# Performance work log

Hardware: AMD Instinct MI355X
Metric: run time of the kernel (lower is better)

Reference implementation:

```python
import jax, jax.numpy as jnp
import numpy as np

N = 50000      # nodes
E = 800000     # directed edges (avg degree 16)
F_IN = 128     # input_size
HID = 128      # hidden_size
OUT = 64       # output_size (bottleneck)
EPS = 1e-5     # BatchNorm eps


def setup_inputs() -> dict:
    key = jax.random.key(0)
    ks = jax.random.split(key, 8)
    x = jax.random.normal(ks[0], (N, F_IN), dtype=jnp.float32)
    edge_index = jax.random.randint(ks[1], (2, E), 0, N, dtype=jnp.int64)
    dims = [(F_IN, HID), (HID, HID), (HID, OUT),   # encoder
            (OUT, HID), (HID, HID), (HID, F_IN)]   # decoder
    wkeys = jax.random.split(ks[2], 6)
    inp = {"x": x, "edge_index": edge_index}
    for j, (fi, fo) in enumerate(dims):
        inp[f"W{j}"] = jax.random.normal(wkeys[j], (fi, fo), dtype=jnp.float32) / np.sqrt(fi).astype(np.float32)
        inp[f"b{j}"] = jnp.zeros((fo,), dtype=jnp.float32)
        inp[f"g{j}"] = jnp.ones((fo,), dtype=jnp.float32)   # BN gamma
        inp[f"be{j}"] = jnp.zeros((fo,), dtype=jnp.float32)  # BN beta
    return inp


def _gcn(x, W, b, src, dst, edge_norm, inv_deg):
    # GCNConv: x' = D^-1/2 (A+I) D^-1/2 (x W) + b, sum-aggregation over edges
    h = x @ W                                   # [N, Fo]
    msg = h[src] * edge_norm[:, None]            # [E, Fo] gather + scale
    agg = jax.ops.segment_sum(msg, dst, num_segments=N)  # scatter-add
    agg = agg + h * inv_deg[:, None]             # self-loop term (norm = 1/deg)
    return agg + b


def _bn(x, g, be):
    # BatchNorm1d over nodes, training-mode batch statistics (biased var)
    m = jnp.mean(x, axis=0)
    v = jnp.mean((x - m) ** 2, axis=0)
    return (x - m) * jax.lax.rsqrt(v + EPS) * g + be


def _forward(x, edge_index, Ws, bs, gs, bes):
    src, dst = edge_index[0], edge_index[1]
    # degrees with self-loops (GCN adds self-loops, counts incoming edges)
    deg = jnp.zeros((N,), dtype=x.dtype).at[dst].add(1.0) + 1.0
    dinv_sqrt = jax.lax.rsqrt(deg)
    edge_norm = dinv_sqrt[src] * dinv_sqrt[dst]
    inv_deg = 1.0 / deg
    h = x
    for j in range(6):
        h = _gcn(h, Ws[j], bs[j], src, dst, edge_norm, inv_deg)
        h = _bn(h, gs[j], bes[j])
        if j not in (2, 5):  # ReLU after first two layers of each GNN, not after bn3
            h = jax.nn.relu(h)
    return h


def reference(x, edge_index,
              W0, b0, g0, be0, W1, b1, g1, be1, W2, b2, g2, be2,
              W3, b3, g3, be3, W4, b4, g4, be4, W5, b5, g5, be5):
    Ws = (W0, W1, W2, W3, W4, W5)
    bs = (b0, b1, b2, b3, b4, b5)
    gs = (g0, g1, g2, g3, g4, g5)
    bes = (be0, be1, be2, be3, be4, be5)
    return _forward(x, edge_index, Ws, bs, gs, bes)
```

## Files before the change

kernel.cpp:

```cpp
#include <hip/hip_runtime.h>
#include <hip/hip_bf16.h>

#define N_NODES 50000
#define N_EDGES 800000
constexpr float BN_EPS = 1e-5f;
constexpr int NCHUNK = (N_NODES + 1023) / 1024;

typedef unsigned short ushortT;

__device__ __forceinline__ unsigned short f2bf(float f) {
    __hip_bfloat16 h = __float2bfloat16(f);
    return __builtin_bit_cast(unsigned short, h);
}
__device__ __forceinline__ void cvt4(uint2 v, float* f) {
    f[0] = __uint_as_float(v.x << 16); f[1] = __uint_as_float(v.x & 0xffff0000u);
    f[2] = __uint_as_float(v.y << 16); f[3] = __uint_as_float(v.y & 0xffff0000u);
}


__global__ void count_deg(const int* __restrict__ dst, int* cnts) {
    int e = blockIdx.x * 256 + threadIdx.x;
    if (e < N_EDGES) atomicAdd(&cnts[dst[e]], 1);
}

__global__ void finalize_deg(const int* __restrict__ cnts, float* __restrict__ dinv,
                             float* __restrict__ invdeg) {
    int i = blockIdx.x * 256 + threadIdx.x;
    if (i < N_NODES) {
        float d = (float)cnts[i] + 1.0f;
        dinv[i] = rsqrtf(d);
        invdeg[i] = 1.0f / d;
    }
}

__global__ __launch_bounds__(256)
void scan_block_sums(const int* __restrict__ counts, int* __restrict__ totals) {
    __shared__ int red[4];
    int tid = threadIdx.x;
    int base = blockIdx.x * 1024 + tid * 4;
    int s = 0;
    #pragma unroll
    for (int j = 0; j < 4; ++j) { int i = base + j; if (i < N_NODES) s += counts[i]; }
    #pragma unroll
    for (int d = 1; d < 64; d <<= 1) s += __shfl_xor(s, d, 64);
    if ((tid & 63) == 0) red[tid >> 6] = s;
    __syncthreads();
    if (tid == 0) totals[blockIdx.x] = red[0] + red[1] + red[2] + red[3];
}

__global__ __launch_bounds__(256)
void scan_write(const int* __restrict__ counts, const int* __restrict__ totals,
                int* __restrict__ offs, int* __restrict__ cursor) {
    __shared__ int chunkbase;
    __shared__ int wsum[4];
    int tid = threadIdx.x, lane = tid & 63, wid = tid >> 6;
    if (tid == 0) { int a = 0; for (int i = 0; i < (int)blockIdx.x; ++i) a += totals[i]; chunkbase = a; }
    int base = blockIdx.x * 1024 + tid * 4;
    int v[4]; int s = 0;
    #pragma unroll
    for (int j = 0; j < 4; ++j) { int i = base + j; v[j] = (i < N_NODES) ? counts[i] : 0; s += v[j]; }
    int ts = s;
    #pragma unroll
    for (int d = 1; d < 64; d <<= 1) { int t = __shfl_up(ts, d, 64); if (lane >= d) ts += t; }
    if (lane == 63) wsum[wid] = ts;
    __syncthreads();
    int wbase = 0;
    #pragma unroll
    for (int w = 0; w < 4; ++w) if (w < wid) wbase += wsum[w];
    int excl = chunkbase + wbase + (ts - s);
    #pragma unroll
    for (int j = 0; j < 4; ++j) {
        int i = base + j;
        if (i < N_NODES) { offs[i] = excl; cursor[i] = excl; }
        excl += v[j];
    }
}

__global__ void fill_csr(const int* __restrict__ src, const int* __restrict__ dst,
                         const float* __restrict__ dinv, int* cursor,
                         uint2* __restrict__ edges) {
    int e = blockIdx.x * 256 + threadIdx.x;
    if (e < N_EDGES) {
        int s = src[e], d = dst[e];
        int pos = atomicAdd(&cursor[d], 1);
        edges[pos] = make_uint2((unsigned)s, __float_as_uint(dinv[s] * dinv[d]));
    }
}


template<int FI, int FO, bool BN, bool RELU>
__global__ __launch_bounds__(256)
void gemm_bn(const float* __restrict__ X, const float* __restrict__ W,
             ushortT* __restrict__ Hb, const float* __restrict__ stats_prev,
             const float* __restrict__ g_prev, const float* __restrict__ be_prev) {
    constexpr int CT = FO / 4;
    constexpr int RT = 256 / CT;
    constexpr int ROWS = RT * 4;
    __shared__ ushortT Ws[FI * FO];
    __shared__ float xs[ROWS * FI];
    __shared__ float sscale[FI], sshift[FI];
    if constexpr (BN) {
        if (threadIdx.x < FI) {
            constexpr float invN = 1.0f / (float)N_NODES;
            int k = threadIdx.x;
            float m = stats_prev[k] * invN;
            float var = stats_prev[FI + k] * invN - m * m;
            float is = rsqrtf(var + BN_EPS) * g_prev[k];
            sscale[k] = is;
            sshift[k] = be_prev[k] - m * is;
        }
    }
    for (int i = threadIdx.x * 8; i < FI * FO; i += 256 * 8) {
        float4 w0 = *(const float4*)&W[i];
        float4 w1 = *(const float4*)&W[i + 4];
        ushortT us[8] = { f2bf(w0.x), f2bf(w0.y), f2bf(w0.z), f2bf(w0.w),
                          f2bf(w1.x), f2bf(w1.y), f2bf(w1.z), f2bf(w1.w) };
        *(uint4*)&Ws[i] = *(uint4*)us;
    }
    const int ct = threadIdx.x % CT, rt = threadIdx.x / CT;
    const int col = ct * 4;
    ushortT* Hcol = Hb + (size_t)(col >> 5) * N_NODES * 32 + (col & 31);
    const int ntiles = (N_NODES + ROWS - 1) / ROWS;
    for (int tile = blockIdx.x; tile < ntiles; tile += gridDim.x) {
        const int base = tile * ROWS;
        __syncthreads();
        for (int t = threadIdx.x; t < ROWS * FI / 4; t += 256) {
            int r = t / (FI / 4), k4 = (t % (FI / 4)) * 4;
            int gr = base + r;
            float4 v = (gr < N_NODES) ? *(const float4*)&X[(size_t)gr * FI + k4]
                                      : make_float4(0.f, 0.f, 0.f, 0.f);
            if constexpr (BN) {
                float4 sc = *(const float4*)&sscale[k4];
                float4 sh = *(const float4*)&sshift[k4];
                v.x = fmaf(v.x, sc.x, sh.x); v.y = fmaf(v.y, sc.y, sh.y);
                v.z = fmaf(v.z, sc.z, sh.z); v.w = fmaf(v.w, sc.w, sh.w);
                if constexpr (RELU) {
                    v.x = fmaxf(v.x, 0.f); v.y = fmaxf(v.y, 0.f);
                    v.z = fmaxf(v.z, 0.f); v.w = fmaxf(v.w, 0.f);
                }
            }
            *(float4*)&xs[r * FI + k4] = v;
        }
        __syncthreads();
        float acc[4][4] = {};
        #pragma unroll 2
        for (int k4 = 0; k4 < FI; k4 += 4) {
            float4 xv[4], wv[4];
            #pragma unroll
            for (int ri = 0; ri < 4; ++ri)
                xv[ri] = *(const float4*)&xs[(rt * 4 + ri) * FI + k4];
            #pragma unroll
            for (int j = 0; j < 4; ++j) {
                ushort4 wu = *(const ushort4*)&Ws[(k4 + j) * FO + col];
                wv[j] = make_float4(__uint_as_float((unsigned)wu.x << 16),
                                    __uint_as_float((unsigned)wu.y << 16),
                                    __uint_as_float((unsigned)wu.z << 16),
                                    __uint_as_float((unsigned)wu.w << 16));
            }
            #pragma unroll
            for (int ri = 0; ri < 4; ++ri) {
                #pragma unroll
                for (int j = 0; j < 4; ++j) {
                    float xk = ((const float*)&xv[ri])[j];
                    acc[ri][0] = fmaf(xk, wv[j].x, acc[ri][0]);
                    acc[ri][1] = fmaf(xk, wv[j].y, acc[ri][1]);
                    acc[ri][2] = fmaf(xk, wv[j].z, acc[ri][2]);
                    acc[ri][3] = fmaf(xk, wv[j].w, acc[ri][3]);
                }
            }
        }
        #pragma unroll
        for (int ri = 0; ri < 4; ++ri) {
            int row = base + rt * 4 + ri;
            if (row < N_NODES) {
                ushortT us[4] = { f2bf(acc[ri][0]), f2bf(acc[ri][1]),
                                  f2bf(acc[ri][2]), f2bf(acc[ri][3]) };
                *(ushort4*)&Hcol[(size_t)row * 32] = *(ushort4*)us;
            }
        }
    }
}


template<int FO>
__global__ __launch_bounds__(256)
void aggregate_sliced(const ushortT* __restrict__ Hb, const int* __restrict__ offs,
                      const int* __restrict__ cnt, const uint2* __restrict__ edges,
                      const float* __restrict__ invdeg, const float* __restrict__ bias,
                      float* __restrict__ out, float* __restrict__ stats) {
    constexpr int NPASS = FO / 32;
    constexpr int BPX = 8 / NPASS;
    const int b = blockIdx.x;
    const int pass = (b & 7) / BPX;
    const int bi = (b >> 3) * BPX + (b & 7) % BPX;
    const int NBP = gridDim.x / NPASS;
    const int lt = threadIdx.x & 7;
    const int sub = threadIdx.x >> 3;
    const uint2* S2 = (const uint2*)(Hb + (size_t)pass * N_NODES * 32);
    const int f0 = pass * 32 + lt * 4;
    float bb[4] = { bias[f0], bias[f0 + 1], bias[f0 + 2], bias[f0 + 3] };
    float s[4] = {}, s2[4] = {};
    for (int r = bi * 32 + sub; r < N_NODES; r += NBP * 32) {
        float idg = invdeg[r];
        float a[4], f[4];
        cvt4(S2[(size_t)r * 8 + lt], f);
        #pragma unroll
        for (int j = 0; j < 4; ++j) a[j] = fmaf(f[j], idg, bb[j]);
        int e = offs[r], en = e + cnt[r];
        for (; e < en; ++e) {
            uint2 ed = edges[e];
            float w = __uint_as_float(ed.y);
            float g[4];
            cvt4(S2[(size_t)ed.x * 8 + lt], g);
            #pragma unroll
            for (int j = 0; j < 4; ++j) a[j] = fmaf(g[j], w, a[j]);
        }
        *(float4*)&out[(size_t)r * FO + f0] = make_float4(a[0], a[1], a[2], a[3]);
        #pragma unroll
        for (int j = 0; j < 4; ++j) { s[j] += a[j]; s2[j] += a[j] * a[j]; }
    }
    __shared__ float ls[256][4], ls2[256][4];
    #pragma unroll
    for (int j = 0; j < 4; ++j) { ls[threadIdx.x][j] = s[j]; ls2[threadIdx.x][j] = s2[j]; }
    __syncthreads();
    if (sub == 0) {
        for (int t = 1; t < 32; ++t) {
            #pragma unroll
            for (int j = 0; j < 4; ++j) {
                s[j] += ls[t * 8 + lt][j];
                s2[j] += ls2[t * 8 + lt][j];
            }
        }
        #pragma unroll
        for (int j = 0; j < 4; ++j) {
            atomicAdd(&stats[f0 + j], s[j]);
            atomicAdd(&stats[FO + f0 + j], s2[j]);
        }
    }
}


template<int FO, bool RELU>
__global__ __launch_bounds__(256)
void bn_norm(const float* __restrict__ X, const float* __restrict__ stats,
             const float* __restrict__ g, const float* __restrict__ be,
             float* __restrict__ Y) {
    constexpr float invN = 1.0f / (float)N_NODES;
    const int total4 = N_NODES * FO / 4;
    for (int idx = blockIdx.x * 256 + threadIdx.x; idx < total4; idx += gridDim.x * 256) {
        int o4 = (idx * 4) & (FO - 1);
        float4 x = ((const float4*)X)[idx];
        float y[4];
        #pragma unroll
        for (int j = 0; j < 4; ++j) {
            int o = o4 + j;
            float m = stats[o] * invN;
            float v = stats[FO + o] * invN - m * m;
            float istd = rsqrtf(v + BN_EPS);
            float val = ((&x.x)[j] - m) * istd * g[o] + be[o];
            if (RELU) val = fmaxf(val, 0.f);
            y[j] = val;
        }
        ((float4*)Y)[idx] = make_float4(y[0], y[1], y[2], y[3]);
    }
}


extern "C" void kernel_launch(void* const* d_in, const int* in_sizes, int n_in,
                              void* d_out, int out_size, void* d_ws, size_t ws_size,
                              hipStream_t stream) {
    const float* x  = (const float*)d_in[0];
    const int* ei   = (const int*)d_in[1];
    const int* src  = ei;
    const int* dst  = ei + N_EDGES;

    size_t off = 0;
    auto alloc = [&](size_t bytes) -> void* {
        void* p = (char*)d_ws + off;
        off += (bytes + 255) & ~(size_t)255;
        return p;
    };
    int*     counts = (int*)    alloc((size_t)N_NODES * 4);
    int*     offs   = (int*)    alloc((size_t)N_NODES * 4);
    int*     cursor = (int*)    alloc((size_t)N_NODES * 4);
    int*     totals = (int*)    alloc((size_t)NCHUNK * 4);
    float*   dinv   = (float*)  alloc((size_t)N_NODES * 4);
    float*   invdeg = (float*)  alloc((size_t)N_NODES * 4);
    uint2*   edges  = (uint2*)  alloc((size_t)N_EDGES * 8);
    float*   stats  = (float*)  alloc(6 * 256 * 4);
    ushortT* Hb     = (ushortT*)alloc((size_t)N_NODES * 128 * 2);
    float*   A0     = (float*)  alloc((size_t)N_NODES * 128 * 4);
    float*   A1     = (float*)  alloc((size_t)N_NODES * 128 * 4);

    hipMemsetAsync(counts, 0, (size_t)N_NODES * 4, stream);
    hipMemsetAsync(stats, 0, 6 * 256 * 4, stream);

    count_deg<<<(N_EDGES + 255) / 256, 256, 0, stream>>>(dst, counts);
    finalize_deg<<<(N_NODES + 255) / 256, 256, 0, stream>>>(counts, dinv, invdeg);
    scan_block_sums<<<NCHUNK, 256, 0, stream>>>(counts, totals);
    scan_write<<<NCHUNK, 256, 0, stream>>>(counts, totals, offs, cursor);
    fill_csr<<<(N_EDGES + 255) / 256, 256, 0, stream>>>(src, dst, dinv, cursor, edges);

    const float* W[6]; const float* b[6]; const float* g[6]; const float* be[6];
    for (int j = 0; j < 6; ++j) {
        W[j]  = (const float*)d_in[2 + 4 * j];
        b[j]  = (const float*)d_in[3 + 4 * j];
        g[j]  = (const float*)d_in[4 + 4 * j];
        be[j] = (const float*)d_in[5 + 4 * j];
    }
    float* st[6];
    for (int j = 0; j < 6; ++j) st[j] = stats + j * 256;
    float* dout = (float*)d_out;

    gemm_bn<128, 128, false, false><<<768, 256, 0, stream>>>(x, W[0], Hb, nullptr, nullptr, nullptr);
    aggregate_sliced<128><<<2048, 256, 0, stream>>>(Hb, offs, counts, edges, invdeg, b[0], A0, st[0]);

    gemm_bn<128, 128, true, true><<<768, 256, 0, stream>>>(A0, W[1], Hb, st[0], g[0], be[0]);
    aggregate_sliced<128><<<2048, 256, 0, stream>>>(Hb, offs, counts, edges, invdeg, b[1], A1, st[1]);

    gemm_bn<128, 64, true, true><<<768, 256, 0, stream>>>(A1, W[2], Hb, st[1], g[1], be[1]);
    aggregate_sliced<64><<<2048, 256, 0, stream>>>(Hb, offs, counts, edges, invdeg, b[2], A0, st[2]);

    gemm_bn<64, 128, true, false><<<768, 256, 0, stream>>>(A0, W[3], Hb, st[2], g[2], be[2]);
    aggregate_sliced<128><<<2048, 256, 0, stream>>>(Hb, offs, counts, edges, invdeg, b[3], A1, st[3]);

    gemm_bn<128, 128, true, true><<<768, 256, 0, stream>>>(A1, W[4], Hb, st[3], g[3], be[3]);
    aggregate_sliced<128><<<2048, 256, 0, stream>>>(Hb, offs, counts, edges, invdeg, b[4], A0, st[4]);

    gemm_bn<128, 128, true, true><<<768, 256, 0, stream>>>(A0, W[5], Hb, st[4], g[4], be[4]);
    aggregate_sliced<128><<<2048, 256, 0, stream>>>(Hb, offs, counts, edges, invdeg, b[5], dout, st[5]);
    bn_norm<128, false><<<2048, 256, 0, stream>>>(dout, st[5], g[5], be[5], dout);
}
```

Baseline: 1.014 ms.

## Pin aggregation feature slices to XCCs with dynamic work-stealing node batches

The aggregation kernel now reads the hardware XCC id and assigns each feature slice to a fixed set of XCCs, so each XCC's L2 holds only one bf16 slice of H. Nodes are handed out dynamically in batches of 64 through a per-slice atomic cursor instead of a static grid stride. Each thread now handles 8 features instead of 4, edges are read two at a time with a one-step prefetch, and non-temporal loads and stores are used for streamed data. The BN stats reduction becomes a shared-memory tree. The risks are that correctness depends on the XCC count being a multiple of the slice count, and the extra block barriers and atomics add per-batch overhead.

```diff
diff --git a/kernel.cpp b/kernel.cpp
--- a/kernel.cpp
+++ b/kernel.cpp
@@ -7,14 +7,19 @@
 constexpr int NCHUNK = (N_NODES + 1023) / 1024;
 
 typedef unsigned short ushortT;
+typedef float    fx4 __attribute__((ext_vector_type(4)));
+typedef unsigned ux2 __attribute__((ext_vector_type(2)));
+typedef unsigned ux4 __attribute__((ext_vector_type(4)));
 
 __device__ __forceinline__ unsigned short f2bf(float f) {
     __hip_bfloat16 h = __float2bfloat16(f);
     return __builtin_bit_cast(unsigned short, h);
 }
-__device__ __forceinline__ void cvt4(uint2 v, float* f) {
-    f[0] = __uint_as_float(v.x << 16); f[1] = __uint_as_float(v.x & 0xffff0000u);
-    f[2] = __uint_as_float(v.y << 16); f[3] = __uint_as_float(v.y & 0xffff0000u);
+__device__ __forceinline__ void cvt8v(ux4 v, float* f) {
+    f[0] = __uint_as_float(v[0] << 16); f[1] = __uint_as_float(v[0] & 0xffff0000u);
+    f[2] = __uint_as_float(v[1] << 16); f[3] = __uint_as_float(v[1] & 0xffff0000u);
+    f[4] = __uint_as_float(v[2] << 16); f[5] = __uint_as_float(v[2] & 0xffff0000u);
+    f[6] = __uint_as_float(v[3] << 16); f[7] = __uint_as_float(v[3] & 0xffff0000u);
 }
 
 
@@ -187,54 +192,97 @@
 void aggregate_sliced(const ushortT* __restrict__ Hb, const int* __restrict__ offs,
                       const int* __restrict__ cnt, const uint2* __restrict__ edges,
                       const float* __restrict__ invdeg, const float* __restrict__ bias,
-                      float* __restrict__ out, float* __restrict__ stats) {
+                      float* __restrict__ out, float* __restrict__ stats,
+                      int* __restrict__ cursor) {
     constexpr int NPASS = FO / 32;
-    constexpr int BPX = 8 / NPASS;
-    const int b = blockIdx.x;
-    const int pass = (b & 7) / BPX;
-    const int bi = (b >> 3) * BPX + (b & 7) % BPX;
-    const int NBP = gridDim.x / NPASS;
-    const int lt = threadIdx.x & 7;
-    const int sub = threadIdx.x >> 3;
-    const uint2* S2 = (const uint2*)(Hb + (size_t)pass * N_NODES * 32);
-    const int f0 = pass * 32 + lt * 4;
-    float bb[4] = { bias[f0], bias[f0 + 1], bias[f0 + 2], bias[f0 + 3] };
-    float s[4] = {}, s2[4] = {};
-    for (int r = bi * 32 + sub; r < N_NODES; r += NBP * 32) {
-        float idg = invdeg[r];
-        float a[4], f[4];
-        cvt4(S2[(size_t)r * 8 + lt], f);
-        #pragma unroll
-        for (int j = 0; j < 4; ++j) a[j] = fmaf(f[j], idg, bb[j]);
-        int e = offs[r], en = e + cnt[r];
-        for (; e < en; ++e) {
-            uint2 ed = edges[e];
-            float w = __uint_as_float(ed.y);
-            float g[4];
-            cvt4(S2[(size_t)ed.x * 8 + lt], g);
-            #pragma unroll
-            for (int j = 0; j < 4; ++j) a[j] = fmaf(g[j], w, a[j]);
-        }
-        *(float4*)&out[(size_t)r * FO + f0] = make_float4(a[0], a[1], a[2], a[3]);
-        #pragma unroll
-        for (int j = 0; j < 4; ++j) { s[j] += a[j]; s2[j] += a[j] * a[j]; }
-    }
-    __shared__ float ls[256][4], ls2[256][4];
-    #pragma unroll
-    for (int j = 0; j < 4; ++j) { ls[threadIdx.x][j] = s[j]; ls2[threadIdx.x][j] = s2[j]; }
+    int xcc;
+    asm volatile("s_getreg_b32 %0, hwreg(HW_REG_XCC_ID)" : "=s"(xcc));
+    const int pass = xcc & (NPASS - 1);
+    const int lt = threadIdx.x & 3;
+    const int sub = threadIdx.x >> 2;
+    const ux4* S4 = (const ux4*)(Hb + (size_t)pass * N_NODES * 32);
+    const ux4* E4 = (const ux4*)edges;
+    const int f0 = pass * 32 + lt * 8;
+    float bb[8];
+    #pragma unroll
+    for (int j = 0; j < 8; ++j) bb[j] = bias[f0 + j];
+    float s[8] = {}, s2[8] = {};
+    __shared__ int batch_s;
+    for (;;) {
+        __syncthreads();
+        if (threadIdx.x == 0) batch_s = atomicAdd(cursor + pass, 64);
+        __syncthreads();
+        int base = batch_s;
+        if (base >= N_NODES) break;
+        int r = base + sub;
+        if (r >= N_NODES) continue;
+        float idg = __builtin_nontemporal_load(&invdeg[r]);
+        int eo = __builtin_nontemporal_load(&offs[r]);
+        int ec = __builtin_nontemporal_load(&cnt[r]);
+        float a[8], f[8];
+        cvt8v(S4[(size_t)r * 4 + lt], f);
+        #pragma unroll
+        for (int j = 0; j < 8; ++j) a[j] = fmaf(f[j], idg, bb[j]);
+        int e = eo, en = eo + ec;
+        if ((e & 1) && e < en) {
+            ux2 ed = __builtin_nontemporal_load((const ux2*)&edges[e]);
+            float w = __uint_as_float(ed[1]);
+            cvt8v(S4[(size_t)ed[0] * 4 + lt], f);
+            #pragma unroll
+            for (int j = 0; j < 8; ++j) a[j] = fmaf(f[j], w, a[j]);
+            ++e;
+        }
+        ux4 ednext = {0, 0, 0, 0};
+        if (e + 2 <= en) ednext = __builtin_nontemporal_load(&E4[e >> 1]);
+        while (e + 2 <= en) {
+            ux4 cur = ednext;
+            if (e + 4 <= en) ednext = __builtin_nontemporal_load(&E4[(e >> 1) + 1]);
+            ux4 v0 = S4[(size_t)cur[0] * 4 + lt];
+            ux4 v1 = S4[(size_t)cur[2] * 4 + lt];
+            float w0 = __uint_as_float(cur[1]), w1 = __uint_as_float(cur[3]);
+            float g0[8], g1[8];
+            cvt8v(v0, g0); cvt8v(v1, g1);
+            #pragma unroll
+            for (int j = 0; j < 8; ++j) a[j] = fmaf(g0[j], w0, a[j]);
+            #pragma unroll
+            for (int j = 0; j < 8; ++j) a[j] = fmaf(g1[j], w1, a[j]);
+            e += 2;
+        }
+        if (e < en) {
+            ux2 ed = __builtin_nontemporal_load((const ux2*)&edges[e]);
+            float w = __uint_as_float(ed[1]);
+            cvt8v(S4[(size_t)ed[0] * 4 + lt], f);
+            #pragma unroll
+            for (int j = 0; j < 8; ++j) a[j] = fmaf(f[j], w, a[j]);
+        }
+        fx4 o0 = { a[0], a[1], a[2], a[3] };
+        fx4 o1 = { a[4], a[5], a[6], a[7] };
+        __builtin_nontemporal_store(o0, (fx4*)&out[(size_t)r * FO + f0]);
+        __builtin_nontemporal_store(o1, (fx4*)&out[(size_t)r * FO + f0 + 4]);
+        #pragma unroll
+        for (int j = 0; j < 8; ++j) { s[j] += a[j]; s2[j] += a[j] * a[j]; }
+    }
+    __shared__ float ls[256][8], ls2[256][8];
+    #pragma unroll
+    for (int j = 0; j < 8; ++j) { ls[threadIdx.x][j] = s[j]; ls2[threadIdx.x][j] = s2[j]; }
     __syncthreads();
-    if (sub == 0) {
-        for (int t = 1; t < 32; ++t) {
-            #pragma unroll
-            for (int j = 0; j < 4; ++j) {
-                s[j] += ls[t * 8 + lt][j];
-                s2[j] += ls2[t * 8 + lt][j];
-            }
-        }
-        #pragma unroll
-        for (int j = 0; j < 4; ++j) {
-            atomicAdd(&stats[f0 + j], s[j]);
-            atomicAdd(&stats[FO + f0 + j], s2[j]);
+    #pragma unroll
+    for (int step = 128; step >= 4; step >>= 1) {
+        if (threadIdx.x < step) {
+            #pragma unroll
+            for (int j = 0; j < 8; ++j) {
+                ls[threadIdx.x][j]  += ls[threadIdx.x + step][j];
+                ls2[threadIdx.x][j] += ls2[threadIdx.x + step][j];
+            }
+        }
+        __syncthreads();
+    }
+    if (threadIdx.x < 4) {
+        int fb = pass * 32 + threadIdx.x * 8;
+        #pragma unroll
+        for (int j = 0; j < 8; ++j) {
+            atomicAdd(&stats[fb + j], ls[threadIdx.x][j]);
+            atomicAdd(&stats[FO + fb + j], ls2[threadIdx.x][j]);
         }
     }
 }
@@ -280,20 +328,22 @@
         off += (bytes + 255) & ~(size_t)255;
         return p;
     };
-    int*     counts = (int*)    alloc((size_t)N_NODES * 4);
-    int*     offs   = (int*)    alloc((size_t)N_NODES * 4);
-    int*     cursor = (int*)    alloc((size_t)N_NODES * 4);
-    int*     totals = (int*)    alloc((size_t)NCHUNK * 4);
-    float*   dinv   = (float*)  alloc((size_t)N_NODES * 4);
-    float*   invdeg = (float*)  alloc((size_t)N_NODES * 4);
-    uint2*   edges  = (uint2*)  alloc((size_t)N_EDGES * 8);
-    float*   stats  = (float*)  alloc(6 * 256 * 4);
-    ushortT* Hb     = (ushortT*)alloc((size_t)N_NODES * 128 * 2);
-    float*   A0     = (float*)  alloc((size_t)N_NODES * 128 * 4);
-    float*   A1     = (float*)  alloc((size_t)N_NODES * 128 * 4);
-
-    hipMemsetAsync(counts, 0, (size_t)N_NODES * 4, stream);
-    hipMemsetAsync(stats, 0, 6 * 256 * 4, stream);
+    int*     counts  = (int*)    alloc((size_t)N_NODES * 4);
+    int*     offs    = (int*)    alloc((size_t)N_NODES * 4);
+    int*     cursor  = (int*)    alloc((size_t)N_NODES * 4);
+    int*     totals  = (int*)    alloc((size_t)NCHUNK * 4);
+    float*   dinv    = (float*)  alloc((size_t)N_NODES * 4);
+    float*   invdeg  = (float*)  alloc((size_t)N_NODES * 4);
+    uint2*   edges   = (uint2*)  alloc((size_t)N_EDGES * 8);
+    float*   stats   = (float*)  alloc(6 * 256 * 4);
+    int*     wcurs   = (int*)    alloc(64 * 4);
+    ushortT* Hb      = (ushortT*)alloc((size_t)N_NODES * 128 * 2);
+    float*   A0      = (float*)  alloc((size_t)N_NODES * 128 * 4);
+    float*   A1      = (float*)  alloc((size_t)N_NODES * 128 * 4);
+
+    (void)hipMemsetAsync(counts, 0, (size_t)N_NODES * 4, stream);
+    (void)hipMemsetAsync(stats, 0, 6 * 256 * 4, stream);
+    (void)hipMemsetAsync(wcurs, 0, 64 * 4, stream);
 
     count_deg<<<(N_EDGES + 255) / 256, 256, 0, stream>>>(dst, counts);
     finalize_deg<<<(N_NODES + 255) / 256, 256, 0, stream>>>(counts, dinv, invdeg);
@@ -313,21 +363,21 @@
     float* dout = (float*)d_out;
 
     gemm_bn<128, 128, false, false><<<768, 256, 0, stream>>>(x, W[0], Hb, nullptr, nullptr, nullptr);
-    aggregate_sliced<128><<<2048, 256, 0, stream>>>(Hb, offs, counts, edges, invdeg, b[0], A0, st[0]);
+    aggregate_sliced<128><<<2048, 256, 0, stream>>>(Hb, offs, counts, edges, invdeg, b[0], A0, st[0], wcurs + 0);
 
     gemm_bn<128, 128, true, true><<<768, 256, 0, stream>>>(A0, W[1], Hb, st[0], g[0], be[0]);
-    aggregate_sliced<128><<<2048, 256, 0, stream>>>(Hb, offs, counts, edges, invdeg, b[1], A1, st[1]);
+    aggregate_sliced<128><<<2048, 256, 0, stream>>>(Hb, offs, counts, edges, invdeg, b[1], A1, st[1], wcurs + 8);
 
     gemm_bn<128, 64, true, true><<<768, 256, 0, stream>>>(A1, W[2], Hb, st[1], g[1], be[1]);
-    aggregate_sliced<64><<<2048, 256, 0, stream>>>(Hb, offs, counts, edges, invdeg, b[2], A0, st[2]);
+    aggregate_sliced<64><<<2048, 256, 0, stream>>>(Hb, offs, counts, edges, invdeg, b[2], A0, st[2], wcurs + 16);
 
     gemm_bn<64, 128, true, false><<<768, 256, 0, stream>>>(A0, W[3], Hb, st[2], g[2], be[2]);
-    aggregate_sliced<128><<<2048, 256, 0, stream>>>(Hb, offs, counts, edges, invdeg, b[3], A1, st[3]);
+    aggregate_sliced<128><<<2048, 256, 0, stream>>>(Hb, offs, counts, edges, invdeg, b[3], A1, st[3], wcurs + 24);
 
     gemm_bn<128, 128, true, true><<<768, 256, 0, stream>>>(A1, W[4], Hb, st[3], g[3], be[3]);
-    aggregate_sliced<128><<<2048, 256, 0, stream>>>(Hb, offs, counts, edges, invdeg, b[4], A0, st[4]);
+    aggregate_sliced<128><<<2048, 256, 0, stream>>>(Hb, offs, counts, edges, invdeg, b[4], A0, st[4], wcurs + 32);
 
     gemm_bn<128, 128, true, true><<<768, 256, 0, stream>>>(A0, W[5], Hb, st[4], g[4], be[4]);
-    aggregate_sliced<128><<<2048, 256, 0, stream>>>(Hb, offs, counts, edges, invdeg, b[5], dout, st[5]);
+    aggregate_sliced<128><<<2048, 256, 0, stream>>>(Hb, offs, counts, edges, invdeg, b[5], dout, st[5], wcurs + 40);
     bn_norm<128, false><<<2048, 256, 0, stream>>>(dout, st[5], g[5], be[5], dout);
 }
```

After: 1.446 ms. 42.6% more time.
